# Performance work log

Measured on AMD Instinct MI355X. Metric: run time of the kernel, lower is better.

Reference implementation:

```python
import jax, jax.numpy as jnp
import numpy as np

N_NODES = 50000
N_EDGES = 800000
D_IN = 96
D_EDGE = 32
D_OUT = 96
N_TYPES = 4


def setup_inputs() -> dict:
    key = jax.random.key(0)
    k = jax.random.split(key, 6)
    x = jax.random.normal(k[0], (N_NODES, D_IN), dtype=jnp.float32)
    edge_features = jax.random.normal(k[1], (N_NODES, D_EDGE), dtype=jnp.float32)
    edge_index = jax.random.randint(k[2], (2, N_EDGES), 0, N_NODES, dtype=jnp.int32)
    edge_type = jax.random.randint(k[3], (N_EDGES,), 0, N_TYPES, dtype=jnp.int32)
    # One RelEdgeConv per relation type: Linear(D_IN + D_EDGE -> D_OUT) message fn
    scale = 1.0 / np.sqrt(D_IN + D_EDGE)
    W_msg = jax.random.uniform(k[4], (N_TYPES, D_IN + D_EDGE, D_OUT), jnp.float32, -scale, scale)
    b_msg = jax.random.uniform(k[5], (N_TYPES, D_OUT), jnp.float32, -scale, scale)
    return {"x": x, "edge_features": edge_features, "edge_index": edge_index,
            "edge_type": edge_type, "W_msg": W_msg, "b_msg": b_msg}


def reference(x, edge_features, edge_index, edge_type, W_msg, b_msg):
    # Node-level edge_features (shape[0] == N) -> per-edge relative features
    src, dst = edge_index[0], edge_index[1]
    e = jnp.abs(edge_features[src] - edge_features[dst])          # [E, De]
    feat = jnp.concatenate([x[src], e], axis=-1)                  # [E, Din+De]
    n_nodes = x.shape[0]
    n_types = W_msg.shape[0]

    def per_type(t):
        # relation mask: zero out messages for edges of other types
        mask = (edge_type == t).astype(x.dtype)[:, None]          # [E, 1]
        m = (feat @ W_msg[t] + b_msg[t]) * mask                   # [E, Dout]
        # scatter-add messages to destination nodes
        return jax.ops.segment_sum(m, dst, num_segments=n_nodes)  # [N, Dout]

    out = jnp.stack([per_type(t) for t in range(n_types)])        # [T, N, Dout]
    return out.mean(axis=0)
```

## Files before the change

### kernel.cpp

```cpp
#include <hip/hip_runtime.h>

#define E_EDGES 800000
#define NN 50000
#define D_IN 96
#define D_EDGE 32
#define D_OUT 96
#define KSUM 512
#define SSTRIDE 520
#define NB4 3125
#define ECAP 20
#define NKEYS 200000
#define NBINS 196
#define BINCAP 4608
#define SCATA 400
#define CHUNK 2000
#define CHIT 8
#define BUILD_BLOCKS 512

typedef __attribute__((ext_vector_type(8))) __bf16 bf16x8;
typedef __attribute__((ext_vector_type(4))) float floatx4;

__device__ __forceinline__ float lo16(unsigned int u) {
    return __builtin_bit_cast(float, u << 16);
}
__device__ __forceinline__ float hi16(unsigned int u) {
    return __builtin_bit_cast(float, u & 0xFFFF0000u);
}
__device__ __forceinline__ unsigned int pk2(float a, float b) {
    unsigned short ua = __builtin_bit_cast(unsigned short, (__bf16)a);
    unsigned short ub = __builtin_bit_cast(unsigned short, (__bf16)b);
    return (unsigned int)ua | ((unsigned int)ub << 16);
}

__global__ __launch_bounds__(256) void k_prep(const int* __restrict__ ei,
                                              const int* __restrict__ et,
                                              const float* __restrict__ x,
                                              const float* __restrict__ ef,
                                              const float* __restrict__ Wm,
                                              int* __restrict__ ccnt,
                                              int* __restrict__ CA,
                                              __bf16* __restrict__ WT,
                                              unsigned int* __restrict__ xeb) {
    __shared__ int h[NBINS], base[NBINS], c2[NBINS], gb[NBINS];
    __shared__ uint2 stage[CHUNK];
    int tid = threadIdx.x, bid = blockIdx.x;

    if (bid < SCATA) {
        int e0 = bid * CHUNK;
        for (int i = tid; i < NBINS; i += 256) h[i] = 0;
        __syncthreads();

        unsigned int rec[CHIT];
        int bn[CHIT];
#pragma unroll
        for (int it = 0; it < CHIT; it++) {
            int i = it * 256 + tid;
            bn[it] = -1;
            if (i < CHUNK) {
                int e = e0 + i;
                int dst = ei[E_EDGES + e];
                int ty  = et[e];
                int src = ei[e];
                rec[it] = ((unsigned)src << 10) | ((unsigned)(dst & 255) << 2)
                        | (unsigned)ty;
                int b = dst >> 8;
                bn[it] = b;
                atomicAdd(&h[b], 1);
            }
        }
        __syncthreads();

        if (tid < 64) {
            int lane = tid, carry = 0;
            for (int s = 0; s < NBINS; s += 64) {
                int idx = s + lane;
                int v = (idx < NBINS) ? h[idx] : 0;
                int sc = v;
                for (int d = 1; d < 64; d <<= 1) {
                    int t = __shfl_up(sc, d, 64);
                    if (lane >= d) sc += t;
                }
                if (idx < NBINS) { base[idx] = carry + sc - v; c2[idx] = carry + sc - v; }
                carry += __shfl(sc, 63, 64);
            }
        }
        __syncthreads();

#pragma unroll
        for (int it = 0; it < CHIT; it++) {
            if (bn[it] >= 0) {
                int pos = atomicAdd(&c2[bn[it]], 1);
                stage[pos] = make_uint2(rec[it], (unsigned)bn[it]);
            }
        }
        for (int b = tid; b < NBINS; b += 256)
            gb[b] = h[b] ? atomicAdd(&ccnt[b], h[b]) : 0;
        __syncthreads();

        for (int i = tid; i < CHUNK; i += 256) {
            uint2 s = stage[i];
            int b = (int)s.y;
            int pos = gb[b] + (i - base[b]);
            if (pos < BINCAP) CA[b * BINCAP + pos] = (int)s.x;
        }
    } else {
        int b2 = bid - SCATA;
        int gtid = b2 * 256 + tid;
        int lane = tid & 63, w = tid >> 6;
        for (int n = b2 * 4 + w; n < NN; n += BUILD_BLOCKS * 4) {
            float2 v;
            if (lane < 48) v = *(const float2*)(x  + (size_t)n * D_IN   + 2 * lane);
            else           v = *(const float2*)(ef + (size_t)n * D_EDGE + 2 * (lane - 48));
            xeb[(size_t)n * 64 + lane] = pk2(v.x, v.y);
        }
        for (int i = gtid; i < 96 * KSUM; i += BUILD_BLOCKS * 256) {
            int n = i >> 9, k = i & 511;
            WT[n * KSUM + k] = (__bf16)Wm[(size_t)k * 96 + n];
        }
    }
}

__global__ __launch_bounds__(256) void k_bin(const int* __restrict__ ccnt,
                                             const int* __restrict__ CA,
                                             int* __restrict__ cnt,
                                             int* __restrict__ eb) {
    __shared__ int kcnt[1024];
    int tid = threadIdx.x, c = blockIdx.x;
    for (int i = tid; i < 1024; i += 256) kcnt[i] = 0;
    __syncthreads();

    int m = min(ccnt[c], BINCAP);
    const int* src = CA + c * BINCAP;
    for (int i = tid; i < m; i += 256) {
        unsigned int r = (unsigned)src[i];
        int lk = (int)((r >> 2) & 255) * 4 + (int)(r & 3);
        int rk = atomicAdd(&kcnt[lk], 1);
        int key = c * 1024 + lk;
        if (rk < ECAP && key < NKEYS)
            eb[key * ECAP + rk] = (int)(r >> 10) << 6;
    }
    __syncthreads();
    for (int lk = tid; lk < 1024; lk += 256) {
        int key = c * 1024 + lk;
        if (key < NKEYS) {
            int kc = kcnt[lk];
            cnt[key] = kc;
            int hh = min(kc, ECAP);
            int pp = (hh + 3) & ~3;
            int pv = (c * 256 + (lk >> 2)) << 6;
            for (int rr = hh; rr < pp; rr++) eb[key * ECAP + rr] = pv;
        }
    }
}

__global__ __launch_bounds__(256) void k_fused(const int* __restrict__ cursor,
                                               const int* __restrict__ eb,
                                               const unsigned int* __restrict__ xeb,
                                               const __bf16* __restrict__ WT,
                                               const float* __restrict__ bm,
                                               float* __restrict__ out) {
    __shared__ __align__(16) __bf16 Sl[16][SSTRIDE];
    __shared__ __align__(16) int el[64 * ECAP];
    __shared__ int h[64];

    int tid = threadIdx.x, lane = tid & 63, w = tid >> 6;
    int B = blockIdx.x;

    if (tid < 64) h[tid] = min(cursor[B * 64 + tid], ECAP);
    {
        const int4* s4 = (const int4*)(eb + (size_t)B * (64 * ECAP));
        int4* d4 = (int4*)el;
        for (int i = tid; i < (64 * ECAP) / 4; i += 256) d4[i] = s4[i];
    }
    __syncthreads();

    unsigned int Mmask = (lane >= 48) ? 0x7FFFFFFFu : 0xFFFFFFFFu;
    int quad = lane >> 4, low = lane & 15;

#define EDGE(u, sa, sb) do {                                                   \
        float f0 = lo16(u), f1 = hi16(u);                                      \
        f0 = __builtin_bit_cast(float,                                         \
                 __builtin_bit_cast(unsigned int, f0 - e0) & Mmask);           \
        f1 = __builtin_bit_cast(float,                                         \
                 __builtin_bit_cast(unsigned int, f1 - e1) & Mmask);           \
        sa += f0; sb += f1;                                                    \
    } while (0)

    for (int j = 0; j < 4; j++) {
        int nl = w * 4 + j;
        int n = B * 16 + nl;
        unsigned int up = xeb[(size_t)n * 64 + lane];
        float xd0 = lo16(up), xd1 = hi16(up);
        float e0 = (lane >= 48) ? xd0 : 0.f;
        float e1 = (lane >= 48) ? xd1 : 0.f;
        float xc0 = (lane < 48) ? xd0 : 0.f;
        float xc1 = (lane < 48) ? xd1 : 0.f;
        unsigned int* sp = (unsigned int*)&Sl[nl][0];

        int h0 = h[nl * 4 + 0], h1 = h[nl * 4 + 1];
        int h2 = h[nl * 4 + 2], h3 = h[nl * 4 + 3];
        int p0 = (h0 + 3) & ~3, p1 = (h1 + 3) & ~3;
        int p2 = (h2 + 3) & ~3, p3 = (h3 + 3) & ~3;
        const int* q0 = el + (nl * 4 + 0) * ECAP;
        const int* q1 = q0 + ECAP;
        const int* q2 = q1 + ECAP;
        const int* q3 = q2 + ECAP;
        float sa0 = 0.f, sb0 = 0.f, sa1 = 0.f, sb1 = 0.f;
        float sa2 = 0.f, sb2 = 0.f, sa3 = 0.f, sb3 = 0.f;
        int mx = max(max(p0, p1), max(p2, p3));
        for (int i = 0; i < mx; i += 4) {
            bool o0 = i < p0, o1 = i < p1, o2 = i < p2, o3 = i < p3;
            unsigned int ua0, ua1, ua2, ua3, ub0, ub1, ub2, ub3;
            unsigned int uc0, uc1, uc2, uc3, ue0, ue1, ue2, ue3;
            if (o0) { int4 a = *(const int4*)(q0 + i);
                      ua0 = xeb[a.x + lane]; ua1 = xeb[a.y + lane];
                      ua2 = xeb[a.z + lane]; ua3 = xeb[a.w + lane]; }
            if (o1) { int4 a = *(const int4*)(q1 + i);
                      ub0 = xeb[a.x + lane]; ub1 = xeb[a.y + lane];
                      ub2 = xeb[a.z + lane]; ub3 = xeb[a.w + lane]; }
            if (o2) { int4 a = *(const int4*)(q2 + i);
                      uc0 = xeb[a.x + lane]; uc1 = xeb[a.y + lane];
                      uc2 = xeb[a.z + lane]; uc3 = xeb[a.w + lane]; }
            if (o3) { int4 a = *(const int4*)(q3 + i);
                      ue0 = xeb[a.x + lane]; ue1 = xeb[a.y + lane];
                      ue2 = xeb[a.z + lane]; ue3 = xeb[a.w + lane]; }
            if (o0) { EDGE(ua0, sa0, sb0); EDGE(ua1, sa0, sb0);
                      EDGE(ua2, sa0, sb0); EDGE(ua3, sa0, sb0); }
            if (o1) { EDGE(ub0, sa1, sb1); EDGE(ub1, sa1, sb1);
                      EDGE(ub2, sa1, sb1); EDGE(ub3, sa1, sb1); }
            if (o2) { EDGE(uc0, sa2, sb2); EDGE(uc1, sa2, sb2);
                      EDGE(uc2, sa2, sb2); EDGE(uc3, sa2, sb2); }
            if (o3) { EDGE(ue0, sa3, sb3); EDGE(ue1, sa3, sb3);
                      EDGE(ue2, sa3, sb3); EDGE(ue3, sa3, sb3); }
        }
        sa0 = fmaf((float)(h0 - p0), xc0, sa0); sb0 = fmaf((float)(h0 - p0), xc1, sb0);
        sa1 = fmaf((float)(h1 - p1), xc0, sa1); sb1 = fmaf((float)(h1 - p1), xc1, sb1);
        sa2 = fmaf((float)(h2 - p2), xc0, sa2); sb2 = fmaf((float)(h2 - p2), xc1, sb2);
        sa3 = fmaf((float)(h3 - p3), xc0, sa3); sb3 = fmaf((float)(h3 - p3), xc1, sb3);
        sp[0 * 64 + lane] = pk2(sa0, sb0);
        sp[1 * 64 + lane] = pk2(sa1, sb1);
        sp[2 * 64 + lane] = pk2(sa2, sb2);
        sp[3 * 64 + lane] = pk2(sa3, sb3);
    }
#undef EDGE
    __syncthreads();

    bf16x8 a[16];
    const __bf16* ap = &Sl[low][0] + quad * 8;
#pragma unroll
    for (int ks = 0; ks < 16; ks++) a[ks] = *(const bf16x8*)(ap + ks * 32);

    for (int ct = w; ct < 6; ct += 4) {
        floatx4 acc = {0.f, 0.f, 0.f, 0.f};
        const __bf16* bp = WT + (size_t)(ct * 16 + low) * KSUM + quad * 8;
#pragma unroll
        for (int ks = 0; ks < 16; ks++)
            acc = __builtin_amdgcn_mfma_f32_16x16x32_bf16(
                a[ks], *(const bf16x8*)(bp + ks * 32), acc, 0, 0, 0);
        int col = ct * 16 + low;
#pragma unroll
        for (int rg = 0; rg < 4; rg++) {
            int r = quad * 4 + rg;
            int g = B * 16 + r;
            float bias = (float)h[r * 4 + 0] * bm[col]
                       + (float)h[r * 4 + 1] * bm[96 + col]
                       + (float)h[r * 4 + 2] * bm[192 + col]
                       + (float)h[r * 4 + 3] * bm[288 + col];
            out[(size_t)g * D_OUT + col] = 0.25f * (acc[rg] + bias);
        }
    }
}

extern "C" void kernel_launch(void* const* d_in, const int* in_sizes, int n_in,
                              void* d_out, int out_size, void* d_ws, size_t ws_size,
                              hipStream_t stream) {
    const float* x  = (const float*)d_in[0];
    const float* ef = (const float*)d_in[1];
    const int*   ei = (const int*)d_in[2];
    const int*   et = (const int*)d_in[3];
    const float* Wm = (const float*)d_in[4];
    const float* bm = (const float*)d_in[5];
    float* out = (float*)d_out;

    int* ccnt = (int*)d_ws;
    int* cnt  = ccnt + 256;
    int* CA   = cnt + NKEYS;
    int* eb   = CA + NBINS * BINCAP;
    __bf16* WT  = (__bf16*)(eb + NKEYS * ECAP);
    unsigned int* xeb = (unsigned int*)(WT + 96 * KSUM);

    hipMemsetAsync(ccnt, 0, NBINS * sizeof(int), stream);
    k_prep <<<SCATA + BUILD_BLOCKS, 256, 0, stream>>>(ei, et, x, ef, Wm,
                                                      ccnt, CA, WT, xeb);
    k_bin  <<<NBINS, 256, 0, stream>>>(ccnt, CA, cnt, eb);
    k_fused<<<NB4, 256, 0, stream>>>(cnt, eb, xeb, WT, bm, out);
}
```

Before: 179.5 us.

## Split fused gather+MFMA kernel into separate gather and matmul kernels

Splits the fused kernel in two. The new gather kernel assigns one node per wave across NN/4 blocks and writes per-node, per-type bf16 aggregates to a global buffer. A second kernel loads that buffer and runs the MFMA projection with the bias term. This aims to raise parallelism and latency hiding in the gather phase, which was serialized over 4 nodes per wave. The cost is an extra kernel launch and a round trip of the aggregates (about 50 MB) through global memory.

```diff
diff --git a/kernel.cpp b/kernel.cpp
--- a/kernel.cpp
+++ b/kernel.cpp
@@ -6,7 +6,6 @@
 #define D_EDGE 32
 #define D_OUT 96
 #define KSUM 512
-#define SSTRIDE 520
 #define NB4 3125
 #define ECAP 20
 #define NKEYS 200000
@@ -153,29 +152,43 @@
     }
 }
 
-__global__ __launch_bounds__(256) void k_fused(const int* __restrict__ cursor,
-                                               const int* __restrict__ eb,
-                                               const unsigned int* __restrict__ xeb,
-                                               const __bf16* __restrict__ WT,
-                                               const float* __restrict__ bm,
-                                               float* __restrict__ out) {
-    __shared__ __align__(16) __bf16 Sl[16][SSTRIDE];
-    __shared__ __align__(16) int el[64 * ECAP];
-    __shared__ int h[64];
-
+__global__ __launch_bounds__(256) void k_gath(const int* __restrict__ cnt,
+                                              const int* __restrict__ eb,
+                                              const unsigned int* __restrict__ xeb,
+                                              unsigned int* __restrict__ Sg) {
+    __shared__ __align__(16) int elw[320];
     int tid = threadIdx.x, lane = tid & 63, w = tid >> 6;
-    int B = blockIdx.x;
-
-    if (tid < 64) h[tid] = min(cursor[B * 64 + tid], ECAP);
+    int bid = blockIdx.x;
+
     {
-        const int4* s4 = (const int4*)(eb + (size_t)B * (64 * ECAP));
-        int4* d4 = (int4*)el;
-        for (int i = tid; i < (64 * ECAP) / 4; i += 256) d4[i] = s4[i];
-    }
+        const int4* s4 = (const int4*)(eb + (size_t)bid * 320);
+        int4* d4 = (int4*)elw;
+        if (tid < 80) d4[tid] = s4[tid];
+    }
+
+    int n = bid * 4 + w;
+    int4 hv = *(const int4*)(cnt + n * 4);
+    int h0 = min(__builtin_amdgcn_readfirstlane(hv.x), ECAP);
+    int h1 = min(__builtin_amdgcn_readfirstlane(hv.y), ECAP);
+    int h2 = min(__builtin_amdgcn_readfirstlane(hv.z), ECAP);
+    int h3 = min(__builtin_amdgcn_readfirstlane(hv.w), ECAP);
+    int p0 = (h0 + 3) & ~3, p1 = (h1 + 3) & ~3;
+    int p2 = (h2 + 3) & ~3, p3 = (h3 + 3) & ~3;
+
+    unsigned int up = xeb[(size_t)n * 64 + lane];
+    float xd0 = lo16(up), xd1 = hi16(up);
+    float e0 = (lane >= 48) ? xd0 : 0.f;
+    float e1 = (lane >= 48) ? xd1 : 0.f;
+    float xc0 = (lane < 48) ? xd0 : 0.f;
+    float xc1 = (lane < 48) ? xd1 : 0.f;
+    unsigned int Mmask = (lane >= 48) ? 0x7FFFFFFFu : 0xFFFFFFFFu;
+
     __syncthreads();
 
-    unsigned int Mmask = (lane >= 48) ? 0x7FFFFFFFu : 0xFFFFFFFFu;
-    int quad = lane >> 4, low = lane & 15;
+    const int* q0 = elw + w * 80;
+    const int* q1 = q0 + ECAP;
+    const int* q2 = q1 + ECAP;
+    const int* q3 = q2 + ECAP;
 
 #define EDGE(u, sa, sb) do {                                                   \
         float f0 = lo16(u), f1 = hi16(u);                                      \
@@ -186,67 +199,58 @@
         sa += f0; sb += f1;                                                    \
     } while (0)
 
-    for (int j = 0; j < 4; j++) {
-        int nl = w * 4 + j;
-        int n = B * 16 + nl;
-        unsigned int up = xeb[(size_t)n * 64 + lane];
-        float xd0 = lo16(up), xd1 = hi16(up);
-        float e0 = (lane >= 48) ? xd0 : 0.f;
-        float e1 = (lane >= 48) ? xd1 : 0.f;
-        float xc0 = (lane < 48) ? xd0 : 0.f;
-        float xc1 = (lane < 48) ? xd1 : 0.f;
-        unsigned int* sp = (unsigned int*)&Sl[nl][0];
-
-        int h0 = h[nl * 4 + 0], h1 = h[nl * 4 + 1];
-        int h2 = h[nl * 4 + 2], h3 = h[nl * 4 + 3];
-        int p0 = (h0 + 3) & ~3, p1 = (h1 + 3) & ~3;
-        int p2 = (h2 + 3) & ~3, p3 = (h3 + 3) & ~3;
-        const int* q0 = el + (nl * 4 + 0) * ECAP;
-        const int* q1 = q0 + ECAP;
-        const int* q2 = q1 + ECAP;
-        const int* q3 = q2 + ECAP;
-        float sa0 = 0.f, sb0 = 0.f, sa1 = 0.f, sb1 = 0.f;
-        float sa2 = 0.f, sb2 = 0.f, sa3 = 0.f, sb3 = 0.f;
-        int mx = max(max(p0, p1), max(p2, p3));
-        for (int i = 0; i < mx; i += 4) {
-            bool o0 = i < p0, o1 = i < p1, o2 = i < p2, o3 = i < p3;
-            unsigned int ua0, ua1, ua2, ua3, ub0, ub1, ub2, ub3;
-            unsigned int uc0, uc1, uc2, uc3, ue0, ue1, ue2, ue3;
-            if (o0) { int4 a = *(const int4*)(q0 + i);
-                      ua0 = xeb[a.x + lane]; ua1 = xeb[a.y + lane];
-                      ua2 = xeb[a.z + lane]; ua3 = xeb[a.w + lane]; }
-            if (o1) { int4 a = *(const int4*)(q1 + i);
-                      ub0 = xeb[a.x + lane]; ub1 = xeb[a.y + lane];
-                      ub2 = xeb[a.z + lane]; ub3 = xeb[a.w + lane]; }
-            if (o2) { int4 a = *(const int4*)(q2 + i);
-                      uc0 = xeb[a.x + lane]; uc1 = xeb[a.y + lane];
-                      uc2 = xeb[a.z + lane]; uc3 = xeb[a.w + lane]; }
-            if (o3) { int4 a = *(const int4*)(q3 + i);
-                      ue0 = xeb[a.x + lane]; ue1 = xeb[a.y + lane];
-                      ue2 = xeb[a.z + lane]; ue3 = xeb[a.w + lane]; }
-            if (o0) { EDGE(ua0, sa0, sb0); EDGE(ua1, sa0, sb0);
-                      EDGE(ua2, sa0, sb0); EDGE(ua3, sa0, sb0); }
-            if (o1) { EDGE(ub0, sa1, sb1); EDGE(ub1, sa1, sb1);
-                      EDGE(ub2, sa1, sb1); EDGE(ub3, sa1, sb1); }
-            if (o2) { EDGE(uc0, sa2, sb2); EDGE(uc1, sa2, sb2);
-                      EDGE(uc2, sa2, sb2); EDGE(uc3, sa2, sb2); }
-            if (o3) { EDGE(ue0, sa3, sb3); EDGE(ue1, sa3, sb3);
-                      EDGE(ue2, sa3, sb3); EDGE(ue3, sa3, sb3); }
-        }
-        sa0 = fmaf((float)(h0 - p0), xc0, sa0); sb0 = fmaf((float)(h0 - p0), xc1, sb0);
-        sa1 = fmaf((float)(h1 - p1), xc0, sa1); sb1 = fmaf((float)(h1 - p1), xc1, sb1);
-        sa2 = fmaf((float)(h2 - p2), xc0, sa2); sb2 = fmaf((float)(h2 - p2), xc1, sb2);
-        sa3 = fmaf((float)(h3 - p3), xc0, sa3); sb3 = fmaf((float)(h3 - p3), xc1, sb3);
-        sp[0 * 64 + lane] = pk2(sa0, sb0);
-        sp[1 * 64 + lane] = pk2(sa1, sb1);
-        sp[2 * 64 + lane] = pk2(sa2, sb2);
-        sp[3 * 64 + lane] = pk2(sa3, sb3);
+    float sa0 = 0.f, sb0 = 0.f, sa1 = 0.f, sb1 = 0.f;
+    float sa2 = 0.f, sb2 = 0.f, sa3 = 0.f, sb3 = 0.f;
+    int mx = max(max(p0, p1), max(p2, p3));
+    for (int i = 0; i < mx; i += 4) {
+        bool o0 = i < p0, o1 = i < p1, o2 = i < p2, o3 = i < p3;
+        unsigned int ua0, ua1, ua2, ua3, ub0, ub1, ub2, ub3;
+        unsigned int uc0, uc1, uc2, uc3, ue0, ue1, ue2, ue3;
+        if (o0) { int4 a = *(const int4*)(q0 + i);
+                  ua0 = xeb[a.x + lane]; ua1 = xeb[a.y + lane];
+                  ua2 = xeb[a.z + lane]; ua3 = xeb[a.w + lane]; }
+        if (o1) { int4 a = *(const int4*)(q1 + i);
+                  ub0 = xeb[a.x + lane]; ub1 = xeb[a.y + lane];
+                  ub2 = xeb[a.z + lane]; ub3 = xeb[a.w + lane]; }
+        if (o2) { int4 a = *(const int4*)(q2 + i);
+                  uc0 = xeb[a.x + lane]; uc1 = xeb[a.y + lane];
+                  uc2 = xeb[a.z + lane]; uc3 = xeb[a.w + lane]; }
+        if (o3) { int4 a = *(const int4*)(q3 + i);
+                  ue0 = xeb[a.x + lane]; ue1 = xeb[a.y + lane];
+                  ue2 = xeb[a.z + lane]; ue3 = xeb[a.w + lane]; }
+        if (o0) { EDGE(ua0, sa0, sb0); EDGE(ua1, sa0, sb0);
+                  EDGE(ua2, sa0, sb0); EDGE(ua3, sa0, sb0); }
+        if (o1) { EDGE(ub0, sa1, sb1); EDGE(ub1, sa1, sb1);
+                  EDGE(ub2, sa1, sb1); EDGE(ub3, sa1, sb1); }
+        if (o2) { EDGE(uc0, sa2, sb2); EDGE(uc1, sa2, sb2);
+                  EDGE(uc2, sa2, sb2); EDGE(uc3, sa2, sb2); }
+        if (o3) { EDGE(ue0, sa3, sb3); EDGE(ue1, sa3, sb3);
+                  EDGE(ue2, sa3, sb3); EDGE(ue3, sa3, sb3); }
     }
 #undef EDGE
-    __syncthreads();
+    sa0 = fmaf((float)(h0 - p0), xc0, sa0); sb0 = fmaf((float)(h0 - p0), xc1, sb0);
+    sa1 = fmaf((float)(h1 - p1), xc0, sa1); sb1 = fmaf((float)(h1 - p1), xc1, sb1);
+    sa2 = fmaf((float)(h2 - p2), xc0, sa2); sb2 = fmaf((float)(h2 - p2), xc1, sb2);
+    sa3 = fmaf((float)(h3 - p3), xc0, sa3); sb3 = fmaf((float)(h3 - p3), xc1, sb3);
+
+    unsigned int* sp = Sg + (size_t)n * 256;
+    sp[0 * 64 + lane] = pk2(sa0, sb0);
+    sp[1 * 64 + lane] = pk2(sa1, sb1);
+    sp[2 * 64 + lane] = pk2(sa2, sb2);
+    sp[3 * 64 + lane] = pk2(sa3, sb3);
+}
+
+__global__ __launch_bounds__(256) void k_mm(const unsigned int* __restrict__ Sg,
+                                            const int* __restrict__ cnt,
+                                            const __bf16* __restrict__ WT,
+                                            const float* __restrict__ bm,
+                                            float* __restrict__ out) {
+    int tid = threadIdx.x, lane = tid & 63, w = tid >> 6;
+    int B = blockIdx.x;
+    int quad = lane >> 4, low = lane & 15;
 
     bf16x8 a[16];
-    const __bf16* ap = &Sl[low][0] + quad * 8;
+    const __bf16* ap = (const __bf16*)Sg + (size_t)(B * 16 + low) * KSUM + quad * 8;
 #pragma unroll
     for (int ks = 0; ks < 16; ks++) a[ks] = *(const bf16x8*)(ap + ks * 32);
 
@@ -262,10 +266,11 @@
         for (int rg = 0; rg < 4; rg++) {
             int r = quad * 4 + rg;
             int g = B * 16 + r;
-            float bias = (float)h[r * 4 + 0] * bm[col]
-                       + (float)h[r * 4 + 1] * bm[96 + col]
-                       + (float)h[r * 4 + 2] * bm[192 + col]
-                       + (float)h[r * 4 + 3] * bm[288 + col];
+            int4 hv = *(const int4*)(cnt + g * 4);
+            float bias = (float)min(hv.x, ECAP) * bm[col]
+                       + (float)min(hv.y, ECAP) * bm[96 + col]
+                       + (float)min(hv.z, ECAP) * bm[192 + col]
+                       + (float)min(hv.w, ECAP) * bm[288 + col];
             out[(size_t)g * D_OUT + col] = 0.25f * (acc[rg] + bias);
         }
     }
@@ -288,10 +293,12 @@
     int* eb   = CA + NBINS * BINCAP;
     __bf16* WT  = (__bf16*)(eb + NKEYS * ECAP);
     unsigned int* xeb = (unsigned int*)(WT + 96 * KSUM);
+    unsigned int* Sg  = xeb + (size_t)NN * 64;
 
     hipMemsetAsync(ccnt, 0, NBINS * sizeof(int), stream);
     k_prep <<<SCATA + BUILD_BLOCKS, 256, 0, stream>>>(ei, et, x, ef, Wm,
                                                       ccnt, CA, WT, xeb);
     k_bin  <<<NBINS, 256, 0, stream>>>(ccnt, CA, cnt, eb);
-    k_fused<<<NB4, 256, 0, stream>>>(cnt, eb, xeb, WT, bm, out);
-}
+    k_gath <<<NN / 4, 256, 0, stream>>>(cnt, eb, xeb, Sg);
+    k_mm   <<<NB4, 256, 0, stream>>>(Sg, cnt, WT, bm, out);
+}
```

Measured after the change: 212.5 us. +18.4%, slower.
